# Optimization experiments

Hardware: AMD Instinct MI355X
Metric: run time of the kernel (lower is better)

Reference implementation:

```python
import jax, jax.numpy as jnp
import numpy as np

EPS = 1e-08
IN_CH = 256
OUT_CH = 256
STYLE_DIM = 256
B, N = 4, 65536


def setup_inputs() -> dict:
    key = jax.random.key(0)
    k1, k2, k3, k4 = jax.random.split(key, 4)
    x = jax.random.normal(k1, (B, N, IN_CH), dtype=jnp.float32)
    style = jax.random.normal(k2, (B, N, STYLE_DIM), dtype=jnp.float32)
    # base weight: torch.randn(1,1,in,out) * sqrt(2/(1+0.2^2)) / sqrt(in)
    w_scale = np.sqrt(2.0 / (1.0 + 0.2 ** 2)) / np.sqrt(IN_CH)
    weight = jax.random.normal(k3, (IN_CH, OUT_CH), dtype=jnp.float32) * w_scale
    bias = jnp.zeros((OUT_CH,), dtype=jnp.float32)
    # affine Linear(style_dim -> in_channel), kaiming normal fan_in linear: std = 1/sqrt(fan_in)
    affine_w = jax.random.normal(k4, (IN_CH, STYLE_DIM), dtype=jnp.float32) / np.sqrt(STYLE_DIM)
    affine_b = jnp.zeros((IN_CH,), dtype=jnp.float32)
    return {"x": x, "style": style, "weight": weight, "bias": bias,
            "affine_w": affine_w, "affine_b": affine_b}


def reference(x, style, weight, bias, affine_w, affine_b):
    # mod[b,n,i] = affine(style) + 1
    mod = jnp.einsum('bns,is->bni', style, affine_w) + affine_b + 1.0
    # out0[b,n,o] = sum_i x[b,n,i] * mod[b,n,i] * weight[i,o]
    out0 = jnp.einsum('bni,io->bno', x * mod, weight)
    # demod[b,n,o] = rsqrt(sum_i (weight[i,o]*mod[b,n,i])^2 + eps)
    ssq = jnp.einsum('bni,io->bno', mod * mod, weight * weight)  # [B,N,out]
    out = out0 * jax.lax.rsqrt(ssq + EPS)
    return out + bias
```

## Files before the change

kernel.cpp:

```cpp
#include <hip/hip_runtime.h>


#define CH   256
#define BM   64
#define NT   16
#define EPS  1e-8f

typedef __attribute__((ext_vector_type(4))) float f32x4;
typedef __attribute__((ext_vector_type(8))) short bf16x8;
typedef __attribute__((ext_vector_type(4))) short s16x4;

__device__ __forceinline__ short f2b(float f) {
    __bf16 h = (__bf16)f;
    return __builtin_bit_cast(short, h);
}
__device__ __forceinline__ float b2f(short b) {
    union { unsigned u; float f; } v;
    v.u = ((unsigned)(unsigned short)b) << 16;
    return v.f;
}
__device__ __forceinline__ int swz(int row, int chunk) {
    return row * 512 + ((chunk ^ (row & 7)) << 4);
}
__device__ __forceinline__ void lds_dma16(const float* g, float* l) {
    __builtin_amdgcn_global_load_lds(
        (const __attribute__((address_space(1))) unsigned int*)g,
        (__attribute__((address_space(3))) unsigned int*)l, 16, 0, 0);
}

__global__ void prep_kernel(const float* __restrict__ weight,
                            const float* __restrict__ affw,
                            short* __restrict__ wTb, short* __restrict__ wT2b,
                            short* __restrict__ affwb)
{
    int t = threadIdx.x, b = blockIdx.x;
    float w  = weight[t * CH + b];
    short wb = f2b(w);
    float wf = b2f(wb);
    wTb  [b * CH + t] = wb;
    wT2b [b * CH + t] = f2b(wf * wf);
    affwb[b * CH + t] = f2b(affw[b * CH + t]);
}

__global__ __launch_bounds__(512, 2)
void smod_main(const float* __restrict__ x, const float* __restrict__ style,
               const float* __restrict__ bias, const float* __restrict__ affb,
               const short* __restrict__ wTb, const short* __restrict__ wT2b,
               const short* __restrict__ affwb,
               float* __restrict__ out)
{
    __shared__ __align__(16) unsigned char smem[131072];
    float* sty = (float*)smem;
    char*  A_s = (char*)smem + 65536;
    char*  B_s = (char*)smem + 98304;
    float* st  = (float*)(smem + 65536);

    const int tid  = threadIdx.x;
    const int lane = tid & 63;
    const int wid  = tid >> 6;
    const int l15  = lane & 15;
    const int lgrp = lane >> 4;
    const int koff = lgrp << 3;
    const long rblk = (long)blockIdx.x * (BM * NT);

    {
        const float* sp = style + rblk * CH;
        #pragma unroll
        for (int k = 0; k < 8; ++k) {
            int seg = wid * 8 + k;
            lds_dma16(sp + seg * 256 + lane * 4, sty + seg * 256);
        }
    }

    #pragma unroll 1
    for (int t = 0; t < NT; ++t) {
        const long r0 = rblk + (long)t * BM;

        asm volatile("s_waitcnt vmcnt(0)" ::: "memory");
        __syncthreads();

        f32x4 xld[4][2];
        #pragma unroll
        for (int k = 0; k < 4; ++k) {
            int u = (k << 9) + tid;
            int row = u >> 5, ch = u & 31;
            const float* p = x + (r0 + row) * CH + ch * 8;
            xld[k][0] = *(const f32x4*)p;
            xld[k][1] = *(const f32x4*)(p + 4);
        }

        #pragma unroll
        for (int k = 0; k < 8; ++k) {
            int u = (k << 9) + tid;
            int row = u >> 6, c4 = u & 63;
            f32x4 v = *(const f32x4*)(sty + row * 256 + c4 * 4);
            s16x4 o = { f2b(v[0]), f2b(v[1]), f2b(v[2]), f2b(v[3]) };
            *(s16x4*)(A_s + swz(row, c4 >> 1) + ((c4 & 1) << 3)) = o;
        }
        __syncthreads();

        if (t + 1 < NT) {
            const float* sp = style + (rblk + (long)(t + 1) * BM) * CH;
            #pragma unroll
            for (int k = 0; k < 8; ++k) {
                int seg = wid * 8 + k;
                lds_dma16(sp + seg * 256 + lane * 4, sty + seg * 256);
            }
        }

        f32x4 accm[2][4];
        #pragma unroll
        for (int a = 0; a < 2; ++a)
            #pragma unroll
            for (int b = 0; b < 4; ++b) { accm[a][b][0]=0.f; accm[a][b][1]=0.f; accm[a][b][2]=0.f; accm[a][b][3]=0.f; }

        #pragma unroll
        for (int kc = 0; kc < 8; ++kc) {
            bf16x8 af[2];
            #pragma unroll
            for (int it = 0; it < 2; ++it)
                af[it] = *(const bf16x8*)(affwb + (wid * 32 + it * 16 + l15) * CH + kc * 32 + koff);
            #pragma unroll
            for (int rt = 0; rt < 4; ++rt) {
                bf16x8 bfr = *(const bf16x8*)(A_s + swz(rt * 16 + l15, kc * 4 + lgrp));
                #pragma unroll
                for (int it = 0; it < 2; ++it)
                    accm[it][rt] = __builtin_amdgcn_mfma_f32_16x16x32_bf16(
                        af[it], bfr, accm[it][rt], 0, 0, 0);
            }
        }
        #pragma unroll
        for (int it = 0; it < 2; ++it) {
            int i0 = wid * 32 + it * 16 + (lgrp << 2);
            f32x4 ab = *(const f32x4*)(affb + i0);
            int chunk = i0 >> 3;
            int sub   = (i0 & 7) << 1;
            #pragma unroll
            for (int rt = 0; rt < 4; ++rt) {
                int row = rt * 16 + l15;
                f32x4 m = accm[it][rt];
                s16x4 o4 = { f2b(m[0] + ab[0] + 1.0f), f2b(m[1] + ab[1] + 1.0f),
                             f2b(m[2] + ab[2] + 1.0f), f2b(m[3] + ab[3] + 1.0f) };
                *(s16x4*)(B_s + swz(row, chunk) + sub) = o4;
            }
        }
        __syncthreads();

        #pragma unroll
        for (int k = 0; k < 4; ++k) {
            int u = (k << 9) + tid;
            int row = u >> 5, ch = u & 31;
            bf16x8 mb = *(const bf16x8*)(B_s + swz(row, ch));
            bf16x8 a1v, a2v;
            #pragma unroll
            for (int j = 0; j < 8; ++j) {
                float mf = b2f(mb[j]);
                float xf = (j < 4) ? xld[k][0][j] : xld[k][1][j - 4];
                a1v[j] = f2b(xf * mf);
                a2v[j] = f2b(mf * mf);
            }
            *(bf16x8*)(A_s + swz(row, ch)) = a1v;
            *(bf16x8*)(B_s + swz(row, ch)) = a2v;
        }
        __syncthreads();

        f32x4 acc0[4][2], acc1[4][2];
        #pragma unroll
        for (int a = 0; a < 4; ++a)
            #pragma unroll
            for (int b = 0; b < 2; ++b) {
                acc0[a][b][0]=0.f; acc0[a][b][1]=0.f; acc0[a][b][2]=0.f; acc0[a][b][3]=0.f;
                acc1[a][b][0]=0.f; acc1[a][b][1]=0.f; acc1[a][b][2]=0.f; acc1[a][b][3]=0.f;
            }

        #pragma unroll
        for (int kc = 0; kc < 8; ++kc) {
            bf16x8 bw[2], bw2[2];
            #pragma unroll
            for (int ct = 0; ct < 2; ++ct) {
                int o = wid * 32 + ct * 16 + l15;
                bw [ct] = *(const bf16x8*)(wTb  + o * CH + kc * 32 + koff);
                bw2[ct] = *(const bf16x8*)(wT2b + o * CH + kc * 32 + koff);
            }
            #pragma unroll
            for (int rt = 0; rt < 4; ++rt) {
                bf16x8 a1f = *(const bf16x8*)(A_s + swz(rt * 16 + l15, kc * 4 + lgrp));
                bf16x8 a2f = *(const bf16x8*)(B_s + swz(rt * 16 + l15, kc * 4 + lgrp));
                #pragma unroll
                for (int ct = 0; ct < 2; ++ct) {
                    acc0[rt][ct] = __builtin_amdgcn_mfma_f32_16x16x32_bf16(
                        a1f, bw[ct],  acc0[rt][ct], 0, 0, 0);
                    acc1[rt][ct] = __builtin_amdgcn_mfma_f32_16x16x32_bf16(
                        a2f, bw2[ct], acc1[rt][ct], 0, 0, 0);
                }
            }
        }
        __syncthreads();

        #pragma unroll
        for (int ct = 0; ct < 2; ++ct) {
            int o = wid * 32 + ct * 16 + l15;
            float bsv = bias[o];
            #pragma unroll
            for (int rt = 0; rt < 4; ++rt)
                #pragma unroll
                for (int j = 0; j < 4; ++j) {
                    int row = rt * 16 + (lgrp << 2) + j;
                    st[row * 256 + o] = acc0[rt][ct][j] * rsqrtf(acc1[rt][ct][j] + EPS) + bsv;
                }
        }
        __syncthreads();

        #pragma unroll
        for (int k = 0; k < 8; ++k) {
            int u = (k << 9) + tid;
            int row = u >> 6, c4 = u & 63;
            f32x4 v = *(const f32x4*)(st + row * 256 + c4 * 4);
            *(f32x4*)(out + (r0 + row) * CH + c4 * 4) = v;
        }
    }
}

extern "C" void kernel_launch(void* const* d_in, const int* in_sizes, int n_in,
                              void* d_out, int out_size, void* d_ws, size_t ws_size,
                              hipStream_t stream) {
    const float* x      = (const float*)d_in[0];
    const float* style  = (const float*)d_in[1];
    const float* weight = (const float*)d_in[2];
    const float* bias   = (const float*)d_in[3];
    const float* affw   = (const float*)d_in[4];
    const float* affb   = (const float*)d_in[5];
    float* outp = (float*)d_out;

    short* ws    = (short*)d_ws;
    short* wTb   = ws;
    short* wT2b  = ws + CH * CH;
    short* affwb = ws + 2 * CH * CH;

    prep_kernel<<<dim3(CH), dim3(CH), 0, stream>>>(weight, affw, wTb, wT2b, affwb);

    smod_main<<<dim3(256), dim3(512), 0, stream>>>(
        x, style, bias, affb, wTb, wT2b, affwb, outp);
}
```

Before: 353.3 us.

## Drop persistent style-DMA pipeline for one-tile-per-block grid with halved LDS

Replaces the persistent 256-block kernel, which looped over 16 tiles and prefetched style into LDS via DMA, with one 64-row tile per block on a 4096-block grid. LDS drops from 128KB to 64KB and launch bounds are raised to allow more resident blocks, so latency is hidden by occupancy rather than an explicit prefetch. Weight fragments are double-buffered in registers across k-chunks. The output GEMM runs in two 32-row halves that reuse the A/B LDS regions for staging results, which cuts accumulator registers but adds barriers. The tighter register budget may cause spills.

```diff
diff --git a/kernel.cpp b/kernel.cpp
--- a/kernel.cpp
+++ b/kernel.cpp
@@ -3,7 +3,6 @@
 
 #define CH   256
 #define BM   64
-#define NT   16
 #define EPS  1e-8f
 
 typedef __attribute__((ext_vector_type(4))) float f32x4;
@@ -21,11 +20,6 @@
 }
 __device__ __forceinline__ int swz(int row, int chunk) {
     return row * 512 + ((chunk ^ (row & 7)) << 4);
-}
-__device__ __forceinline__ void lds_dma16(const float* g, float* l) {
-    __builtin_amdgcn_global_load_lds(
-        (const __attribute__((address_space(1))) unsigned int*)g,
-        (__attribute__((address_space(3))) unsigned int*)l, 16, 0, 0);
 }
 
 __global__ void prep_kernel(const float* __restrict__ weight,
@@ -42,18 +36,16 @@
     affwb[b * CH + t] = f2b(affw[b * CH + t]);
 }
 
-__global__ __launch_bounds__(512, 2)
+__global__ __launch_bounds__(512, 4)
 void smod_main(const float* __restrict__ x, const float* __restrict__ style,
                const float* __restrict__ bias, const float* __restrict__ affb,
                const short* __restrict__ wTb, const short* __restrict__ wT2b,
                const short* __restrict__ affwb,
                float* __restrict__ out)
 {
-    __shared__ __align__(16) unsigned char smem[131072];
-    float* sty = (float*)smem;
-    char*  A_s = (char*)smem + 65536;
-    char*  B_s = (char*)smem + 98304;
-    float* st  = (float*)(smem + 65536);
+    __shared__ __align__(16) unsigned char smem[65536];
+    char* A_s = (char*)smem;
+    char* B_s = (char*)smem + 32768;
 
     const int tid  = threadIdx.x;
     const int lane = tid & 63;
@@ -61,163 +53,228 @@
     const int l15  = lane & 15;
     const int lgrp = lane >> 4;
     const int koff = lgrp << 3;
-    const long rblk = (long)blockIdx.x * (BM * NT);
-
-    {
-        const float* sp = style + rblk * CH;
-        #pragma unroll
-        for (int k = 0; k < 8; ++k) {
-            int seg = wid * 8 + k;
-            lds_dma16(sp + seg * 256 + lane * 4, sty + seg * 256);
-        }
-    }
-
-    #pragma unroll 1
-    for (int t = 0; t < NT; ++t) {
-        const long r0 = rblk + (long)t * BM;
-
-        asm volatile("s_waitcnt vmcnt(0)" ::: "memory");
-        __syncthreads();
-
-        f32x4 xld[4][2];
-        #pragma unroll
-        for (int k = 0; k < 4; ++k) {
-            int u = (k << 9) + tid;
-            int row = u >> 5, ch = u & 31;
-            const float* p = x + (r0 + row) * CH + ch * 8;
-            xld[k][0] = *(const f32x4*)p;
-            xld[k][1] = *(const f32x4*)(p + 4);
-        }
-
-        #pragma unroll
-        for (int k = 0; k < 8; ++k) {
-            int u = (k << 9) + tid;
-            int row = u >> 6, c4 = u & 63;
-            f32x4 v = *(const f32x4*)(sty + row * 256 + c4 * 4);
-            s16x4 o = { f2b(v[0]), f2b(v[1]), f2b(v[2]), f2b(v[3]) };
-            *(s16x4*)(A_s + swz(row, c4 >> 1) + ((c4 & 1) << 3)) = o;
-        }
-        __syncthreads();
-
-        if (t + 1 < NT) {
-            const float* sp = style + (rblk + (long)(t + 1) * BM) * CH;
-            #pragma unroll
-            for (int k = 0; k < 8; ++k) {
-                int seg = wid * 8 + k;
-                lds_dma16(sp + seg * 256 + lane * 4, sty + seg * 256);
-            }
-        }
-
-        f32x4 accm[2][4];
-        #pragma unroll
-        for (int a = 0; a < 2; ++a)
-            #pragma unroll
-            for (int b = 0; b < 4; ++b) { accm[a][b][0]=0.f; accm[a][b][1]=0.f; accm[a][b][2]=0.f; accm[a][b][3]=0.f; }
-
-        #pragma unroll
-        for (int kc = 0; kc < 8; ++kc) {
-            bf16x8 af[2];
+    const long r0  = (long)blockIdx.x * BM;
+
+    auto strow = [&](int r) -> char* {
+        return (char*)smem + ((r >> 4) & 1) * 32768 + (r >> 5) * 16384 + (r & 15) * 1024;
+    };
+
+    #pragma unroll
+    for (int k = 0; k < 8; ++k) {
+        int u = (k << 9) + tid;
+        int row = u >> 6, c4 = u & 63;
+        f32x4 v = *(const f32x4*)(style + (r0 + row) * CH + c4 * 4);
+        s16x4 o4 = { f2b(v[0]), f2b(v[1]), f2b(v[2]), f2b(v[3]) };
+        *(s16x4*)(A_s + swz(row, c4 >> 1) + ((c4 & 1) << 3)) = o4;
+    }
+    __syncthreads();
+
+    f32x4 accm[2][4];
+    #pragma unroll
+    for (int a = 0; a < 2; ++a)
+        #pragma unroll
+        for (int b = 0; b < 4; ++b) { accm[a][b][0]=0.f; accm[a][b][1]=0.f; accm[a][b][2]=0.f; accm[a][b][3]=0.f; }
+
+    bf16x8 af_a[2], af_b[2];
+    #pragma unroll
+    for (int it = 0; it < 2; ++it)
+        af_a[it] = *(const bf16x8*)(affwb + (wid * 32 + it * 16 + l15) * CH + 0 + koff);
+
+    #pragma unroll
+    for (int kc = 0; kc < 8; ++kc) {
+        if (kc < 7) {
+            #pragma unroll
+            for (int it = 0; it < 2; ++it) {
+                bf16x8 v = *(const bf16x8*)(affwb + (wid * 32 + it * 16 + l15) * CH + (kc + 1) * 32 + koff);
+                if (kc & 1) af_a[it] = v; else af_b[it] = v;
+            }
+        }
+        #pragma unroll
+        for (int rt = 0; rt < 4; ++rt) {
+            bf16x8 bfr = *(const bf16x8*)(A_s + swz(rt * 16 + l15, kc * 4 + lgrp));
             #pragma unroll
             for (int it = 0; it < 2; ++it)
-                af[it] = *(const bf16x8*)(affwb + (wid * 32 + it * 16 + l15) * CH + kc * 32 + koff);
-            #pragma unroll
-            for (int rt = 0; rt < 4; ++rt) {
-                bf16x8 bfr = *(const bf16x8*)(A_s + swz(rt * 16 + l15, kc * 4 + lgrp));
-                #pragma unroll
-                for (int it = 0; it < 2; ++it)
-                    accm[it][rt] = __builtin_amdgcn_mfma_f32_16x16x32_bf16(
-                        af[it], bfr, accm[it][rt], 0, 0, 0);
-            }
-        }
-        #pragma unroll
-        for (int it = 0; it < 2; ++it) {
-            int i0 = wid * 32 + it * 16 + (lgrp << 2);
-            f32x4 ab = *(const f32x4*)(affb + i0);
-            int chunk = i0 >> 3;
-            int sub   = (i0 & 7) << 1;
-            #pragma unroll
-            for (int rt = 0; rt < 4; ++rt) {
-                int row = rt * 16 + l15;
-                f32x4 m = accm[it][rt];
-                s16x4 o4 = { f2b(m[0] + ab[0] + 1.0f), f2b(m[1] + ab[1] + 1.0f),
-                             f2b(m[2] + ab[2] + 1.0f), f2b(m[3] + ab[3] + 1.0f) };
-                *(s16x4*)(B_s + swz(row, chunk) + sub) = o4;
-            }
-        }
-        __syncthreads();
-
-        #pragma unroll
-        for (int k = 0; k < 4; ++k) {
-            int u = (k << 9) + tid;
-            int row = u >> 5, ch = u & 31;
-            bf16x8 mb = *(const bf16x8*)(B_s + swz(row, ch));
-            bf16x8 a1v, a2v;
-            #pragma unroll
-            for (int j = 0; j < 8; ++j) {
-                float mf = b2f(mb[j]);
-                float xf = (j < 4) ? xld[k][0][j] : xld[k][1][j - 4];
-                a1v[j] = f2b(xf * mf);
-                a2v[j] = f2b(mf * mf);
-            }
-            *(bf16x8*)(A_s + swz(row, ch)) = a1v;
-            *(bf16x8*)(B_s + swz(row, ch)) = a2v;
-        }
-        __syncthreads();
-
-        f32x4 acc0[4][2], acc1[4][2];
-        #pragma unroll
-        for (int a = 0; a < 4; ++a)
-            #pragma unroll
-            for (int b = 0; b < 2; ++b) {
-                acc0[a][b][0]=0.f; acc0[a][b][1]=0.f; acc0[a][b][2]=0.f; acc0[a][b][3]=0.f;
-                acc1[a][b][0]=0.f; acc1[a][b][1]=0.f; acc1[a][b][2]=0.f; acc1[a][b][3]=0.f;
-            }
-
-        #pragma unroll
-        for (int kc = 0; kc < 8; ++kc) {
-            bf16x8 bw[2], bw2[2];
+                accm[it][rt] = __builtin_amdgcn_mfma_f32_16x16x32_bf16(
+                    (kc & 1) ? af_b[it] : af_a[it], bfr, accm[it][rt], 0, 0, 0);
+        }
+    }
+
+    f32x4 xld[8];
+    #pragma unroll
+    for (int k = 0; k < 8; ++k) {
+        int u = (k << 9) + tid;
+        int row = u >> 6, q = u & 63;
+        xld[k] = *(const f32x4*)(x + (r0 + row) * CH + q * 4);
+    }
+
+    #pragma unroll
+    for (int it = 0; it < 2; ++it) {
+        int i0 = wid * 32 + it * 16 + (lgrp << 2);
+        f32x4 ab = *(const f32x4*)(affb + i0);
+        int chunk = i0 >> 3;
+        int sub   = (i0 & 7) << 1;
+        #pragma unroll
+        for (int rt = 0; rt < 4; ++rt) {
+            int row = rt * 16 + l15;
+            f32x4 m = accm[it][rt];
+            s16x4 o4 = { f2b(m[0] + ab[0] + 1.0f), f2b(m[1] + ab[1] + 1.0f),
+                         f2b(m[2] + ab[2] + 1.0f), f2b(m[3] + ab[3] + 1.0f) };
+            *(s16x4*)(B_s + swz(row, chunk) + sub) = o4;
+        }
+    }
+    __syncthreads();
+
+    #pragma unroll
+    for (int k = 0; k < 8; ++k) {
+        int u = (k << 9) + tid;
+        int row = u >> 6, q = u & 63;
+        int boff = swz(row, q >> 1) + ((q & 1) << 3);
+        s16x4 mb = *(const s16x4*)(B_s + boff);
+        f32x4 xv = xld[k];
+        s16x4 a1v, a2v;
+        #pragma unroll
+        for (int j = 0; j < 4; ++j) {
+            float mf = b2f(mb[j]);
+            a1v[j] = f2b(xv[j] * mf);
+            a2v[j] = f2b(mf * mf);
+        }
+        *(s16x4*)(A_s + boff) = a1v;
+        *(s16x4*)(B_s + boff) = a2v;
+    }
+    __syncthreads();
+
+    f32x4 acc0[2][2], acc1[2][2];
+    bf16x8 bw_a[2], bw2_a[2], bw_b[2], bw2_b[2];
+    #pragma unroll
+    for (int a = 0; a < 2; ++a)
+        #pragma unroll
+        for (int b = 0; b < 2; ++b) {
+            acc0[a][b][0]=0.f; acc0[a][b][1]=0.f; acc0[a][b][2]=0.f; acc0[a][b][3]=0.f;
+            acc1[a][b][0]=0.f; acc1[a][b][1]=0.f; acc1[a][b][2]=0.f; acc1[a][b][3]=0.f;
+        }
+    #pragma unroll
+    for (int ct = 0; ct < 2; ++ct) {
+        int o = wid * 32 + ct * 16 + l15;
+        bw_a [ct] = *(const bf16x8*)(wTb  + o * CH + koff);
+        bw2_a[ct] = *(const bf16x8*)(wT2b + o * CH + koff);
+    }
+    #pragma unroll
+    for (int kc = 0; kc < 8; ++kc) {
+        if (kc < 7) {
             #pragma unroll
             for (int ct = 0; ct < 2; ++ct) {
                 int o = wid * 32 + ct * 16 + l15;
-                bw [ct] = *(const bf16x8*)(wTb  + o * CH + kc * 32 + koff);
-                bw2[ct] = *(const bf16x8*)(wT2b + o * CH + kc * 32 + koff);
-            }
-            #pragma unroll
-            for (int rt = 0; rt < 4; ++rt) {
-                bf16x8 a1f = *(const bf16x8*)(A_s + swz(rt * 16 + l15, kc * 4 + lgrp));
-                bf16x8 a2f = *(const bf16x8*)(B_s + swz(rt * 16 + l15, kc * 4 + lgrp));
-                #pragma unroll
-                for (int ct = 0; ct < 2; ++ct) {
-                    acc0[rt][ct] = __builtin_amdgcn_mfma_f32_16x16x32_bf16(
-                        a1f, bw[ct],  acc0[rt][ct], 0, 0, 0);
-                    acc1[rt][ct] = __builtin_amdgcn_mfma_f32_16x16x32_bf16(
-                        a2f, bw2[ct], acc1[rt][ct], 0, 0, 0);
-                }
-            }
-        }
-        __syncthreads();
-
-        #pragma unroll
-        for (int ct = 0; ct < 2; ++ct) {
-            int o = wid * 32 + ct * 16 + l15;
-            float bsv = bias[o];
-            #pragma unroll
-            for (int rt = 0; rt < 4; ++rt)
-                #pragma unroll
-                for (int j = 0; j < 4; ++j) {
-                    int row = rt * 16 + (lgrp << 2) + j;
-                    st[row * 256 + o] = acc0[rt][ct][j] * rsqrtf(acc1[rt][ct][j] + EPS) + bsv;
-                }
-        }
-        __syncthreads();
-
-        #pragma unroll
-        for (int k = 0; k < 8; ++k) {
-            int u = (k << 9) + tid;
-            int row = u >> 6, c4 = u & 63;
-            f32x4 v = *(const f32x4*)(st + row * 256 + c4 * 4);
-            *(f32x4*)(out + (r0 + row) * CH + c4 * 4) = v;
-        }
+                bf16x8 v1 = *(const bf16x8*)(wTb  + o * CH + (kc + 1) * 32 + koff);
+                bf16x8 v2 = *(const bf16x8*)(wT2b + o * CH + (kc + 1) * 32 + koff);
+                if (kc & 1) { bw_a[ct] = v1; bw2_a[ct] = v2; }
+                else        { bw_b[ct] = v1; bw2_b[ct] = v2; }
+            }
+        }
+        bf16x8 a1f[2], a2f[2];
+        #pragma unroll
+        for (int rt = 0; rt < 2; ++rt) {
+            a1f[rt] = *(const bf16x8*)(A_s + swz(rt * 16 + l15, kc * 4 + lgrp));
+            a2f[rt] = *(const bf16x8*)(B_s + swz(rt * 16 + l15, kc * 4 + lgrp));
+        }
+        #pragma unroll
+        for (int rt = 0; rt < 2; ++rt)
+            #pragma unroll
+            for (int ct = 0; ct < 2; ++ct) {
+                acc0[rt][ct] = __builtin_amdgcn_mfma_f32_16x16x32_bf16(
+                    a1f[rt], (kc & 1) ? bw_b[ct]  : bw_a[ct],  acc0[rt][ct], 0, 0, 0);
+                acc1[rt][ct] = __builtin_amdgcn_mfma_f32_16x16x32_bf16(
+                    a2f[rt], (kc & 1) ? bw2_b[ct] : bw2_a[ct], acc1[rt][ct], 0, 0, 0);
+            }
+    }
+    __syncthreads();
+
+    #pragma unroll
+    for (int ct = 0; ct < 2; ++ct) {
+        int o = wid * 32 + ct * 16 + l15;
+        float bsv = bias[o];
+        #pragma unroll
+        for (int rt = 0; rt < 2; ++rt)
+            #pragma unroll
+            for (int j = 0; j < 4; ++j) {
+                int r = rt * 16 + (lgrp << 2) + j;
+                *(float*)(strow(r) + o * 4) =
+                    acc0[rt][ct][j] * rsqrtf(acc1[rt][ct][j] + EPS) + bsv;
+            }
+    }
+    __syncthreads();
+
+    #pragma unroll
+    for (int k = 0; k < 4; ++k) {
+        int u = (k << 9) + tid;
+        int row = u >> 6, c4 = u & 63;
+        f32x4 v = *(const f32x4*)(strow(row) + c4 * 16);
+        *(f32x4*)(out + (r0 + row) * CH + c4 * 4) = v;
+    }
+
+    #pragma unroll
+    for (int a = 0; a < 2; ++a)
+        #pragma unroll
+        for (int b = 0; b < 2; ++b) {
+            acc0[a][b][0]=0.f; acc0[a][b][1]=0.f; acc0[a][b][2]=0.f; acc0[a][b][3]=0.f;
+            acc1[a][b][0]=0.f; acc1[a][b][1]=0.f; acc1[a][b][2]=0.f; acc1[a][b][3]=0.f;
+        }
+    #pragma unroll
+    for (int ct = 0; ct < 2; ++ct) {
+        int o = wid * 32 + ct * 16 + l15;
+        bw_a [ct] = *(const bf16x8*)(wTb  + o * CH + koff);
+        bw2_a[ct] = *(const bf16x8*)(wT2b + o * CH + koff);
+    }
+    #pragma unroll
+    for (int kc = 0; kc < 8; ++kc) {
+        if (kc < 7) {
+            #pragma unroll
+            for (int ct = 0; ct < 2; ++ct) {
+                int o = wid * 32 + ct * 16 + l15;
+                bf16x8 v1 = *(const bf16x8*)(wTb  + o * CH + (kc + 1) * 32 + koff);
+                bf16x8 v2 = *(const bf16x8*)(wT2b + o * CH + (kc + 1) * 32 + koff);
+                if (kc & 1) { bw_a[ct] = v1; bw2_a[ct] = v2; }
+                else        { bw_b[ct] = v1; bw2_b[ct] = v2; }
+            }
+        }
+        bf16x8 a1f[2], a2f[2];
+        #pragma unroll
+        for (int rt = 0; rt < 2; ++rt) {
+            a1f[rt] = *(const bf16x8*)(A_s + swz(32 + rt * 16 + l15, kc * 4 + lgrp));
+            a2f[rt] = *(const bf16x8*)(B_s + swz(32 + rt * 16 + l15, kc * 4 + lgrp));
+        }
+        #pragma unroll
+        for (int rt = 0; rt < 2; ++rt)
+            #pragma unroll
+            for (int ct = 0; ct < 2; ++ct) {
+                acc0[rt][ct] = __builtin_amdgcn_mfma_f32_16x16x32_bf16(
+                    a1f[rt], (kc & 1) ? bw_b[ct]  : bw_a[ct],  acc0[rt][ct], 0, 0, 0);
+                acc1[rt][ct] = __builtin_amdgcn_mfma_f32_16x16x32_bf16(
+                    a2f[rt], (kc & 1) ? bw2_b[ct] : bw2_a[ct], acc1[rt][ct], 0, 0, 0);
+            }
+    }
+    __syncthreads();
+
+    #pragma unroll
+    for (int ct = 0; ct < 2; ++ct) {
+        int o = wid * 32 + ct * 16 + l15;
+        float bsv = bias[o];
+        #pragma unroll
+        for (int rt = 0; rt < 2; ++rt)
+            #pragma unroll
+            for (int j = 0; j < 4; ++j) {
+                int r = 32 + rt * 16 + (lgrp << 2) + j;
+                *(float*)(strow(r) + o * 4) =
+                    acc0[rt][ct][j] * rsqrtf(acc1[rt][ct][j] + EPS) + bsv;
+            }
+    }
+    __syncthreads();
+
+    #pragma unroll
+    for (int k = 0; k < 4; ++k) {
+        int u = (k << 9) + tid;
+        int row = 32 + (u >> 6), c4 = u & 63;
+        f32x4 v = *(const f32x4*)(strow(row) + c4 * 16);
+        *(f32x4*)(out + (r0 + row) * CH + c4 * 4) = v;
     }
 }
 
@@ -239,6 +296,7 @@
 
     prep_kernel<<<dim3(CH), dim3(CH), 0, stream>>>(weight, affw, wTb, wT2b, affwb);
 
-    smod_main<<<dim3(256), dim3(512), 0, stream>>>(
+    const int rows = 4 * 65536;
+    smod_main<<<dim3(rows / BM), dim3(512), 0, stream>>>(
         x, style, bias, affb, wTb, wT2b, affwb, outp);
 }
```

After: 391.0 us. +10.7%, slower.

## Process one 64-row tile per block with halved LDS for higher occupancy

Applied to the files above, without the earlier changes.

Replaces the persistent 16-tile loop (256 blocks, 128KB LDS) with one 64-row tile per block (4096 blocks, 64KB LDS) and launch bounds raised to 4 blocks per CU. The K dimension of the main GEMM is split into two halves so the A/B staging buffers fit in the smaller LDS. The x tile is DMA'd into swizzled LDS in halves, with the second half's load overlapped with the first-half MFMAs. MFMA sections are wrapped in s_setprio. The aim is to hide memory latency through more resident waves rather than through software prefetch across tiles, at the cost of losing the style prefetch and adding extra barriers and launch overhead.

```diff
diff --git a/kernel.cpp b/kernel.cpp
--- a/kernel.cpp
+++ b/kernel.cpp
@@ -3,7 +3,6 @@
 
 #define CH   256
 #define BM   64
-#define NT   16
 #define EPS  1e-8f
 
 typedef __attribute__((ext_vector_type(4))) float f32x4;
@@ -19,8 +18,11 @@
     v.u = ((unsigned)(unsigned short)b) << 16;
     return v.f;
 }
-__device__ __forceinline__ int swz(int row, int chunk) {
-    return row * 512 + ((chunk ^ (row & 7)) << 4);
+__device__ __forceinline__ int swz512(int row, int ch) {
+    return row * 512 + ((ch ^ (row & 7)) << 4);
+}
+__device__ __forceinline__ int swz256(int row, int ch) {
+    return row * 256 + ((ch ^ (row & 7)) << 4);
 }
 __device__ __forceinline__ void lds_dma16(const float* g, float* l) {
     __builtin_amdgcn_global_load_lds(
@@ -42,18 +44,19 @@
     affwb[b * CH + t] = f2b(affw[b * CH + t]);
 }
 
-__global__ __launch_bounds__(512, 2)
+__global__ __launch_bounds__(512, 4)
 void smod_main(const float* __restrict__ x, const float* __restrict__ style,
                const float* __restrict__ bias, const float* __restrict__ affb,
                const short* __restrict__ wTb, const short* __restrict__ wT2b,
                const short* __restrict__ affwb,
                float* __restrict__ out)
 {
-    __shared__ __align__(16) unsigned char smem[131072];
-    float* sty = (float*)smem;
-    char*  A_s = (char*)smem + 65536;
-    char*  B_s = (char*)smem + 98304;
-    float* st  = (float*)(smem + 65536);
+    __shared__ __align__(16) unsigned char smem[65536];
+    char*  sty   = (char*)smem;
+    char*  A_s   = (char*)smem;
+    char*  B_s   = (char*)smem + 16384;
+    float* xland = (float*)(smem + 32768);
+    float* st    = (float*)smem;
 
     const int tid  = threadIdx.x;
     const int lane = tid & 63;
@@ -61,163 +64,216 @@
     const int l15  = lane & 15;
     const int lgrp = lane >> 4;
     const int koff = lgrp << 3;
-    const long rblk = (long)blockIdx.x * (BM * NT);
-
-    {
-        const float* sp = style + rblk * CH;
-        #pragma unroll
-        for (int k = 0; k < 8; ++k) {
-            int seg = wid * 8 + k;
-            lds_dma16(sp + seg * 256 + lane * 4, sty + seg * 256);
-        }
-    }
-
-    #pragma unroll 1
-    for (int t = 0; t < NT; ++t) {
-        const long r0 = rblk + (long)t * BM;
-
-        asm volatile("s_waitcnt vmcnt(0)" ::: "memory");
-        __syncthreads();
-
-        f32x4 xld[4][2];
+    const long r0  = (long)blockIdx.x * BM;
+
+    auto dma_x_half = [&](int h) {
         #pragma unroll
         for (int k = 0; k < 4; ++k) {
-            int u = (k << 9) + tid;
-            int row = u >> 5, ch = u & 31;
-            const float* p = x + (r0 + row) * CH + ch * 8;
-            xld[k][0] = *(const f32x4*)p;
-            xld[k][1] = *(const f32x4*)(p + 4);
-        }
-
-        #pragma unroll
-        for (int k = 0; k < 8; ++k) {
-            int u = (k << 9) + tid;
-            int row = u >> 6, c4 = u & 63;
-            f32x4 v = *(const f32x4*)(sty + row * 256 + c4 * 4);
-            s16x4 o = { f2b(v[0]), f2b(v[1]), f2b(v[2]), f2b(v[3]) };
-            *(s16x4*)(A_s + swz(row, c4 >> 1) + ((c4 & 1) << 3)) = o;
-        }
-        __syncthreads();
-
-        if (t + 1 < NT) {
-            const float* sp = style + (rblk + (long)(t + 1) * BM) * CH;
+            int j   = wid * 4 + k;
+            int row = 2 * j + (lane >> 5);
+            int c   = lane & 31;
+            int scol = ((((c >> 1) ^ (row & 7)) << 3) | ((c & 1) << 2));
+            lds_dma16(x + (r0 + row) * CH + h * 128 + scol, xland + j * 256);
+        }
+    };
+
+    dma_x_half(0);
+
+    #pragma unroll
+    for (int k = 0; k < 8; ++k) {
+        int u = (k << 9) + tid;
+        int row = u >> 6, c4 = u & 63;
+        f32x4 v = *(const f32x4*)(style + (r0 + row) * CH + c4 * 4);
+        s16x4 o4 = { f2b(v[0]), f2b(v[1]), f2b(v[2]), f2b(v[3]) };
+        *(s16x4*)(sty + swz512(row, c4 >> 1) + ((c4 & 1) << 3)) = o4;
+    }
+    __syncthreads();
+
+    f32x4 accm[2][4];
+    #pragma unroll
+    for (int a = 0; a < 2; ++a)
+        #pragma unroll
+        for (int b = 0; b < 4; ++b) { accm[a][b][0]=0.f; accm[a][b][1]=0.f; accm[a][b][2]=0.f; accm[a][b][3]=0.f; }
+
+    #pragma unroll
+    for (int kc = 0; kc < 8; ++kc) {
+        bf16x8 af[2], bfr[4];
+        af[0] = *(const bf16x8*)(affwb + (wid * 16 + l15) * CH + kc * 32 + koff);
+        af[1] = *(const bf16x8*)(affwb + (128 + wid * 16 + l15) * CH + kc * 32 + koff);
+        #pragma unroll
+        for (int rt = 0; rt < 4; ++rt)
+            bfr[rt] = *(const bf16x8*)(sty + swz512(rt * 16 + l15, kc * 4 + lgrp));
+        __builtin_amdgcn_s_setprio(1);
+        #pragma unroll
+        for (int it = 0; it < 2; ++it)
             #pragma unroll
-            for (int k = 0; k < 8; ++k) {
-                int seg = wid * 8 + k;
-                lds_dma16(sp + seg * 256 + lane * 4, sty + seg * 256);
-            }
-        }
-
-        f32x4 accm[2][4];
-        #pragma unroll
-        for (int a = 0; a < 2; ++a)
-            #pragma unroll
-            for (int b = 0; b < 4; ++b) { accm[a][b][0]=0.f; accm[a][b][1]=0.f; accm[a][b][2]=0.f; accm[a][b][3]=0.f; }
-
-        #pragma unroll
-        for (int kc = 0; kc < 8; ++kc) {
-            bf16x8 af[2];
-            #pragma unroll
-            for (int it = 0; it < 2; ++it)
-                af[it] = *(const bf16x8*)(affwb + (wid * 32 + it * 16 + l15) * CH + kc * 32 + koff);
-            #pragma unroll
-            for (int rt = 0; rt < 4; ++rt) {
-                bf16x8 bfr = *(const bf16x8*)(A_s + swz(rt * 16 + l15, kc * 4 + lgrp));
-                #pragma unroll
-                for (int it = 0; it < 2; ++it)
-                    accm[it][rt] = __builtin_amdgcn_mfma_f32_16x16x32_bf16(
-                        af[it], bfr, accm[it][rt], 0, 0, 0);
-            }
-        }
-        #pragma unroll
-        for (int it = 0; it < 2; ++it) {
-            int i0 = wid * 32 + it * 16 + (lgrp << 2);
-            f32x4 ab = *(const f32x4*)(affb + i0);
-            int chunk = i0 >> 3;
-            int sub   = (i0 & 7) << 1;
-            #pragma unroll
-            for (int rt = 0; rt < 4; ++rt) {
-                int row = rt * 16 + l15;
-                f32x4 m = accm[it][rt];
-                s16x4 o4 = { f2b(m[0] + ab[0] + 1.0f), f2b(m[1] + ab[1] + 1.0f),
-                             f2b(m[2] + ab[2] + 1.0f), f2b(m[3] + ab[3] + 1.0f) };
-                *(s16x4*)(B_s + swz(row, chunk) + sub) = o4;
-            }
-        }
-        __syncthreads();
-
-        #pragma unroll
-        for (int k = 0; k < 4; ++k) {
-            int u = (k << 9) + tid;
-            int row = u >> 5, ch = u & 31;
-            bf16x8 mb = *(const bf16x8*)(B_s + swz(row, ch));
-            bf16x8 a1v, a2v;
-            #pragma unroll
-            for (int j = 0; j < 8; ++j) {
-                float mf = b2f(mb[j]);
-                float xf = (j < 4) ? xld[k][0][j] : xld[k][1][j - 4];
-                a1v[j] = f2b(xf * mf);
-                a2v[j] = f2b(mf * mf);
-            }
-            *(bf16x8*)(A_s + swz(row, ch)) = a1v;
-            *(bf16x8*)(B_s + swz(row, ch)) = a2v;
-        }
-        __syncthreads();
-
-        f32x4 acc0[4][2], acc1[4][2];
-        #pragma unroll
-        for (int a = 0; a < 4; ++a)
-            #pragma unroll
-            for (int b = 0; b < 2; ++b) {
-                acc0[a][b][0]=0.f; acc0[a][b][1]=0.f; acc0[a][b][2]=0.f; acc0[a][b][3]=0.f;
-                acc1[a][b][0]=0.f; acc1[a][b][1]=0.f; acc1[a][b][2]=0.f; acc1[a][b][3]=0.f;
-            }
-
-        #pragma unroll
-        for (int kc = 0; kc < 8; ++kc) {
-            bf16x8 bw[2], bw2[2];
+            for (int rt = 0; rt < 4; ++rt)
+                accm[it][rt] = __builtin_amdgcn_mfma_f32_16x16x32_bf16(
+                    af[it], bfr[rt], accm[it][rt], 0, 0, 0);
+        __builtin_amdgcn_s_setprio(0);
+    }
+
+    const int i_lo = wid * 16 + (lgrp << 2);
+    f32x4 ab0 = *(const f32x4*)(affb + i_lo);
+    f32x4 ab1 = *(const f32x4*)(affb + 128 + i_lo);
+    s16x4 modreg[4];
+    #pragma unroll
+    for (int rt = 0; rt < 4; ++rt) {
+        f32x4 m = accm[1][rt];
+        modreg[rt] = s16x4{ f2b(m[0] + ab1[0] + 1.0f), f2b(m[1] + ab1[1] + 1.0f),
+                            f2b(m[2] + ab1[2] + 1.0f), f2b(m[3] + ab1[3] + 1.0f) };
+    }
+    __syncthreads();
+
+    const int mchunk = i_lo >> 3;
+    const int msub   = (i_lo & 7) << 1;
+
+    #pragma unroll
+    for (int rt = 0; rt < 4; ++rt) {
+        int row = rt * 16 + l15;
+        f32x4 m = accm[0][rt];
+        s16x4 o4 = { f2b(m[0] + ab0[0] + 1.0f), f2b(m[1] + ab0[1] + 1.0f),
+                     f2b(m[2] + ab0[2] + 1.0f), f2b(m[3] + ab0[3] + 1.0f) };
+        *(s16x4*)(B_s + swz256(row, mchunk) + msub) = o4;
+    }
+    asm volatile("s_waitcnt vmcnt(0)" ::: "memory");
+    __syncthreads();
+
+    #pragma unroll
+    for (int k = 0; k < 4; ++k) {
+        int u = (k << 9) + tid;
+        int row = u >> 5, c4 = u & 31;
+        int boff = swz256(row, c4 >> 1) + ((c4 & 1) << 3);
+        s16x4 mb = *(const s16x4*)(B_s + boff);
+        f32x4 xv = *(const f32x4*)((char*)xland + row * 512 +
+                                   (((c4 >> 1) ^ (row & 7)) << 5) + ((c4 & 1) << 4));
+        s16x4 a1v, a2v;
+        #pragma unroll
+        for (int j = 0; j < 4; ++j) {
+            float mf = b2f(mb[j]);
+            a1v[j] = f2b(xv[j] * mf);
+            a2v[j] = f2b(mf * mf);
+        }
+        *(s16x4*)(A_s + boff) = a1v;
+        *(s16x4*)(B_s + boff) = a2v;
+    }
+    __syncthreads();
+
+    dma_x_half(1);
+
+    f32x4 acc0[4][2], acc1[4][2];
+    #pragma unroll
+    for (int a = 0; a < 4; ++a)
+        #pragma unroll
+        for (int b = 0; b < 2; ++b) {
+            acc0[a][b][0]=0.f; acc0[a][b][1]=0.f; acc0[a][b][2]=0.f; acc0[a][b][3]=0.f;
+            acc1[a][b][0]=0.f; acc1[a][b][1]=0.f; acc1[a][b][2]=0.f; acc1[a][b][3]=0.f;
+        }
+
+    #pragma unroll
+    for (int kc = 0; kc < 4; ++kc) {
+        bf16x8 bw[2], bw2[2];
+        #pragma unroll
+        for (int ct = 0; ct < 2; ++ct) {
+            int o = wid * 32 + ct * 16 + l15;
+            bw [ct] = *(const bf16x8*)(wTb  + o * CH + kc * 32 + koff);
+            bw2[ct] = *(const bf16x8*)(wT2b + o * CH + kc * 32 + koff);
+        }
+        bf16x8 a1f[4], a2f[4];
+        #pragma unroll
+        for (int rt = 0; rt < 4; ++rt) {
+            a1f[rt] = *(const bf16x8*)(A_s + swz256(rt * 16 + l15, kc * 4 + lgrp));
+            a2f[rt] = *(const bf16x8*)(B_s + swz256(rt * 16 + l15, kc * 4 + lgrp));
+        }
+        __builtin_amdgcn_s_setprio(1);
+        #pragma unroll
+        for (int rt = 0; rt < 4; ++rt)
             #pragma unroll
             for (int ct = 0; ct < 2; ++ct) {
-                int o = wid * 32 + ct * 16 + l15;
-                bw [ct] = *(const bf16x8*)(wTb  + o * CH + kc * 32 + koff);
-                bw2[ct] = *(const bf16x8*)(wT2b + o * CH + kc * 32 + koff);
+                acc0[rt][ct] = __builtin_amdgcn_mfma_f32_16x16x32_bf16(
+                    a1f[rt], bw[ct],  acc0[rt][ct], 0, 0, 0);
+                acc1[rt][ct] = __builtin_amdgcn_mfma_f32_16x16x32_bf16(
+                    a2f[rt], bw2[ct], acc1[rt][ct], 0, 0, 0);
             }
-            #pragma unroll
-            for (int rt = 0; rt < 4; ++rt) {
-                bf16x8 a1f = *(const bf16x8*)(A_s + swz(rt * 16 + l15, kc * 4 + lgrp));
-                bf16x8 a2f = *(const bf16x8*)(B_s + swz(rt * 16 + l15, kc * 4 + lgrp));
-                #pragma unroll
-                for (int ct = 0; ct < 2; ++ct) {
-                    acc0[rt][ct] = __builtin_amdgcn_mfma_f32_16x16x32_bf16(
-                        a1f, bw[ct],  acc0[rt][ct], 0, 0, 0);
-                    acc1[rt][ct] = __builtin_amdgcn_mfma_f32_16x16x32_bf16(
-                        a2f, bw2[ct], acc1[rt][ct], 0, 0, 0);
-                }
-            }
-        }
-        __syncthreads();
-
+        __builtin_amdgcn_s_setprio(0);
+    }
+    __syncthreads();
+
+    #pragma unroll
+    for (int rt = 0; rt < 4; ++rt)
+        *(s16x4*)(B_s + swz256(rt * 16 + l15, mchunk) + msub) = modreg[rt];
+    asm volatile("s_waitcnt vmcnt(0)" ::: "memory");
+    __syncthreads();
+
+    #pragma unroll
+    for (int k = 0; k < 4; ++k) {
+        int u = (k << 9) + tid;
+        int row = u >> 5, c4 = u & 31;
+        int boff = swz256(row, c4 >> 1) + ((c4 & 1) << 3);
+        s16x4 mb = *(const s16x4*)(B_s + boff);
+        f32x4 xv = *(const f32x4*)((char*)xland + row * 512 +
+                                   (((c4 >> 1) ^ (row & 7)) << 5) + ((c4 & 1) << 4));
+        s16x4 a1v, a2v;
+        #pragma unroll
+        for (int j = 0; j < 4; ++j) {
+            float mf = b2f(mb[j]);
+            a1v[j] = f2b(xv[j] * mf);
+            a2v[j] = f2b(mf * mf);
+        }
+        *(s16x4*)(A_s + boff) = a1v;
+        *(s16x4*)(B_s + boff) = a2v;
+    }
+    __syncthreads();
+
+    #pragma unroll
+    for (int kc = 0; kc < 4; ++kc) {
+        bf16x8 bw[2], bw2[2];
         #pragma unroll
         for (int ct = 0; ct < 2; ++ct) {
             int o = wid * 32 + ct * 16 + l15;
-            float bsv = bias[o];
+            bw [ct] = *(const bf16x8*)(wTb  + o * CH + 128 + kc * 32 + koff);
+            bw2[ct] = *(const bf16x8*)(wT2b + o * CH + 128 + kc * 32 + koff);
+        }
+        bf16x8 a1f[4], a2f[4];
+        #pragma unroll
+        for (int rt = 0; rt < 4; ++rt) {
+            a1f[rt] = *(const bf16x8*)(A_s + swz256(rt * 16 + l15, kc * 4 + lgrp));
+            a2f[rt] = *(const bf16x8*)(B_s + swz256(rt * 16 + l15, kc * 4 + lgrp));
+        }
+        __builtin_amdgcn_s_setprio(1);
+        #pragma unroll
+        for (int rt = 0; rt < 4; ++rt)
             #pragma unroll
-            for (int rt = 0; rt < 4; ++rt)
-                #pragma unroll
-                for (int j = 0; j < 4; ++j) {
-                    int row = rt * 16 + (lgrp << 2) + j;
-                    st[row * 256 + o] = acc0[rt][ct][j] * rsqrtf(acc1[rt][ct][j] + EPS) + bsv;
-                }
-        }
-        __syncthreads();
-
-        #pragma unroll
-        for (int k = 0; k < 8; ++k) {
-            int u = (k << 9) + tid;
-            int row = u >> 6, c4 = u & 63;
-            f32x4 v = *(const f32x4*)(st + row * 256 + c4 * 4);
-            *(f32x4*)(out + (r0 + row) * CH + c4 * 4) = v;
-        }
+            for (int ct = 0; ct < 2; ++ct) {
+                acc0[rt][ct] = __builtin_amdgcn_mfma_f32_16x16x32_bf16(
+                    a1f[rt], bw[ct],  acc0[rt][ct], 0, 0, 0);
+                acc1[rt][ct] = __builtin_amdgcn_mfma_f32_16x16x32_bf16(
+                    a2f[rt], bw2[ct], acc1[rt][ct], 0, 0, 0);
+            }
+        __builtin_amdgcn_s_setprio(0);
+    }
+    __syncthreads();
+
+    #pragma unroll
+    for (int ct = 0; ct < 2; ++ct) {
+        int o = wid * 32 + ct * 16 + l15;
+        float bsv = bias[o];
+        #pragma unroll
+        for (int rt = 0; rt < 4; ++rt)
+            #pragma unroll
+            for (int j = 0; j < 4; ++j) {
+                int row = rt * 16 + (lgrp << 2) + j;
+                st[row * 256 + o] = acc0[rt][ct][j] * rsqrtf(acc1[rt][ct][j] + EPS) + bsv;
+            }
+    }
+    __syncthreads();
+
+    #pragma unroll
+    for (int k = 0; k < 8; ++k) {
+        int u = (k << 9) + tid;
+        int row = u >> 6, c4 = u & 63;
+        f32x4 v = *(const f32x4*)(st + row * 256 + c4 * 4);
+        *(f32x4*)(out + (r0 + row) * CH + c4 * 4) = v;
     }
 }
 
@@ -239,6 +295,7 @@
 
     prep_kernel<<<dim3(CH), dim3(CH), 0, stream>>>(weight, affw, wTb, wT2b, affwb);
 
-    smod_main<<<dim3(256), dim3(512), 0, stream>>>(
+    const int rows = 4 * 65536;
+    smod_main<<<dim3(rows / BM), dim3(512), 0, stream>>>(
         x, style, bias, affb, wTb, wT2b, affwb, outp);
 }
```

New measurement: 390.0 us. 10.4% more time.
